# Kernel tuning notes

Hardware: AMD Instinct MI355X
Metric: run time of the kernel (lower is better)

Reference implementation:

```python
import jax, jax.numpy as jnp
import numpy as np

EPS = 1e-12  # torch F.normalize default eps

def _l2_normalize(x):
    # F.normalize(x, dim=1): x / max(||x||_2, eps), per row
    n = jnp.linalg.norm(x, axis=1, keepdims=True)
    return x / jnp.maximum(n, EPS)

def setup_inputs() -> dict:
    key = jax.random.key(0)
    ks = jax.random.split(key, 7)
    B, D = 8192, 4096
    s = 1.0 / np.sqrt(D)  # keep activations well-scaled like nn.Linear init
    return {
        "x":  jax.random.normal(ks[0], (B, D), dtype=jnp.float32),
        "W0": jax.random.normal(ks[1], (D, D), dtype=jnp.float32) * s,
        "b0": jax.random.normal(ks[2], (D,),   dtype=jnp.float32) * s,
        "W1": jax.random.normal(ks[3], (D, D), dtype=jnp.float32) * s,
        "b1": jax.random.normal(ks[4], (D,),   dtype=jnp.float32) * s,
        "W2": jax.random.normal(ks[5], (D, D), dtype=jnp.float32) * s,
        "b2": jax.random.normal(ks[6], (D,),   dtype=jnp.float32) * s,
    }

def reference(x, W0, b0, W1, b1, W2, b2):
    # per layer: out = relu(Linear(l2_normalize(x, dim=1))); collect all layer outputs
    params = [(W0, b0), (W1, b1), (W2, b2)]
    outs = []
    h = x
    for W, b in params:
        hn = _l2_normalize(h)
        # nn.Linear stores weight as [out, in]: y = hn @ W.T + b
        h = jax.nn.relu(jnp.einsum('bi,oi->bo', hn, W) + b)
        outs.append(h)
    return tuple(outs)
```

## Files before the change

### kernel.cpp

```cpp
#include <hip/hip_runtime.h>
#include <hip/hip_bf16.h>


#define NROWS 8192
#define DIM   4096

typedef __bf16 bf16x8 __attribute__((ext_vector_type(8)));
typedef float  f32x4  __attribute__((ext_vector_type(4)));

__device__ static inline short f2bf(float f) {
  __hip_bfloat16 h = __float2bfloat16(f);
  return __builtin_bit_cast(short, h);
}

#define BARRIER() do { asm volatile("" ::: "memory"); \
                       __builtin_amdgcn_s_barrier();  \
                       asm volatile("" ::: "memory"); } while (0)
#define GATE()   do { asm volatile("s_waitcnt lgkmcnt(0)" ::: "memory"); \
                      __builtin_amdgcn_sched_barrier(0); } while (0)
#define VMW(N)   do { asm volatile("s_waitcnt vmcnt(" #N ")" ::: "memory"); \
                      __builtin_amdgcn_sched_barrier(0); } while (0)

__global__ __launch_bounds__(512, 2)
void gemm256_bias_relu(const short* __restrict__ A,
                       const short* __restrict__ Bw,
                       const float* __restrict__ bias,
                       float* __restrict__ C,
                       int M, int N, int K)
{
  __shared__ short lds[5][16384];

  int bid = blockIdx.x;
  const int nwg = gridDim.x;
  if ((nwg & 7) == 0) { const int cpx = nwg >> 3; bid = (bid & 7) * cpx + (bid >> 3); }
  const int nbn  = N >> 8;
  const int brow = (bid / nbn) << 8;
  const int bcol = (bid % nbn) << 8;

  const int lane = threadIdx.x & 63;
  const int wid  = threadIdx.x >> 6;
  const int wr   = wid >> 2;
  const int wc   = wid & 3;

  f32x4 acc[8][4] = {};

  const size_t rowK = (size_t)K * 2;
  char* const  ldsB = (char*)&lds[0][0];

  const int r8  = lane >> 3;
  const int kcs = (lane & 7) ^ r8;
  const char* AgL = (const char*)A  + (size_t)(brow + r8) * rowK + (size_t)kcs * 16;
  const char* BgL = (const char*)Bw + (size_t)(bcol + r8) * rowK + (size_t)kcs * 16;
  int rbo[4], rbb[4];
#pragma unroll
  for (int i = 0; i < 4; ++i) {
    const int rb = wid * 8 + i * 64;
    rbo[i] = rb * (int)rowK;
    rbb[i] = rb * 128;
  }
  auto stage = [&](const char* gsrc, char* lb, int tile) {
    const char* gp = gsrc + ((size_t)tile << 7);
#pragma unroll
    for (int s = 0; s < 4; ++s)
      __builtin_amdgcn_global_load_lds(
          (const __attribute__((address_space(1))) void*)(gp + rbo[s]),
          (__attribute__((address_space(3))) void*)(lb + rbb[s]), 16, 0, 0);
  };

  const int l15  = lane & 15;
  const int xlo  = ((lane >> 4) ^ (lane & 3)) * 16;
  const int b2   = (lane >> 2) & 1;
  const int k64[2] = { b2 << 6, (1 - b2) << 6 };
  const int abase = (wr * 128 + l15) * 128 + xlo;
  const int bbase = (wc * 64  + l15) * 128 + xlo;

  const int NT = K >> 6;

  bf16x8 aX[4][2], aY[4][2], bF[4][2];

#define LOAD_FRAG(DST, PTR, BASE, I0)                                        \
  _Pragma("unroll")                                                          \
  for (int ii = 0; ii < 4; ++ii)                                             \
    _Pragma("unroll")                                                        \
    for (int ks = 0; ks < 2; ++ks)                                           \
      DST[ii][ks] = *reinterpret_cast<const bf16x8*>(                        \
          (PTR) + (BASE) + ((I0) + ii) * 2048 + k64[ks]);

#define MFMA16(I0, AF)                                                       \
  _Pragma("unroll")                                                          \
  for (int ks = 0; ks < 2; ++ks)                                             \
    _Pragma("unroll")                                                        \
    for (int ii = 0; ii < 4; ++ii)                                           \
      _Pragma("unroll")                                                      \
      for (int j = 0; j < 4; ++j)                                            \
        acc[(I0) + ii][j] = __builtin_amdgcn_mfma_f32_16x16x32_bf16(         \
            AF[ii][ks], bF[j][ks], acc[(I0) + ii][j], 0, 0, 0);

  char* a0 = ldsB;
  char* a1 = ldsB + 32768;
  char* a2 = ldsB + 65536;
  char* b0 = ldsB + 98304;
  char* b1 = ldsB + 131072;

  stage(AgL, a0, 0);
  if (NT > 1) stage(AgL, a1, 1);
  stage(BgL, b0, 0);
  if (NT > 1) stage(BgL, b1, 1);
  VMW(0);
  BARRIER();
  LOAD_FRAG(aX, a0, abase, 0)

  for (int t = 0; t < NT; ++t) {
    if (t + 2 < NT) stage(AgL, a2, t + 2);
    LOAD_FRAG(bF, b0, bbase, 0)
    BARRIER();
    GATE();
    LOAD_FRAG(aY, a0, abase, 4)
    __builtin_amdgcn_s_setprio(1);
    MFMA16(0, aX)
    __builtin_amdgcn_s_setprio(0);

    if (t + 2 < NT) { VMW(4); }
    else            { VMW(0); }
    BARRIER();
    GATE();
    if (t + 2 < NT) stage(BgL, b0, t + 2);
    if (t + 1 < NT) { LOAD_FRAG(aX, a1, abase, 0) }
    __builtin_amdgcn_s_setprio(1);
    MFMA16(4, aY)
    __builtin_amdgcn_s_setprio(0);

    char* tmp = a0; a0 = a1; a1 = a2; a2 = tmp;
    char* tb = b0; b0 = b1; b1 = tb;
  }
#undef MFMA16
#undef LOAD_FRAG

  float bv[4];
#pragma unroll
  for (int j = 0; j < 4; ++j)
    bv[j] = bias[bcol + wc * 64 + j * 16 + (lane & 15)];
#pragma unroll
  for (int i = 0; i < 8; ++i) {
    const int rbase = brow + wr * 128 + i * 16 + ((lane >> 4) << 2);
#pragma unroll
    for (int j = 0; j < 4; ++j) {
      const int col = bcol + wc * 64 + j * 16 + (lane & 15);
#pragma unroll
      for (int r = 0; r < 4; ++r) {
        const float v = acc[i][j][r] + bv[j];
        C[(size_t)(rbase + r) * N + col] = v > 0.f ? v : 0.f;
      }
    }
  }
}

__global__ __launch_bounds__(256)
void rownorm_bf16(const float* __restrict__ in, short* __restrict__ out)
{
  const int row = blockIdx.x;
  const int t0  = threadIdx.x;
  const float4* inr = (const float4*)(in + (size_t)row * DIM);

  float4 v[4];
  float ss = 0.f;
#pragma unroll
  for (int t = 0; t < 4; ++t) {
    v[t] = inr[t0 + t * 256];
    ss += v[t].x * v[t].x + v[t].y * v[t].y + v[t].z * v[t].z + v[t].w * v[t].w;
  }
#pragma unroll
  for (int off = 32; off > 0; off >>= 1)
    ss += __shfl_down(ss, off, 64);

  __shared__ float wss[4];
  if ((t0 & 63) == 0) wss[t0 >> 6] = ss;
  __syncthreads();
  const float tot   = wss[0] + wss[1] + wss[2] + wss[3];
  const float scale = 1.f / fmaxf(sqrtf(tot), 1e-12f);

  short4* outr = (short4*)(out + (size_t)row * DIM);
#pragma unroll
  for (int t = 0; t < 4; ++t) {
    short4 o;
    o.x = f2bf(v[t].x * scale);
    o.y = f2bf(v[t].y * scale);
    o.z = f2bf(v[t].z * scale);
    o.w = f2bf(v[t].w * scale);
    outr[t0 + t * 256] = o;
  }
}

__global__ __launch_bounds__(256)
void cast_bf16(const float* __restrict__ in, short* __restrict__ out, int n4)
{
  int i = blockIdx.x * 256 + threadIdx.x;
  const int stride = gridDim.x * 256;
  for (; i < n4; i += stride) {
    const float4 v = ((const float4*)in)[i];
    short4 o;
    o.x = f2bf(v.x);
    o.y = f2bf(v.y);
    o.z = f2bf(v.z);
    o.w = f2bf(v.w);
    ((short4*)out)[i] = o;
  }
}

extern "C" void kernel_launch(void* const* d_in, const int* in_sizes, int n_in,
                              void* d_out, int out_size, void* d_ws, size_t ws_size,
                              hipStream_t stream) {
  const float* x = (const float*)d_in[0];
  const float* W[3]    = { (const float*)d_in[1], (const float*)d_in[3], (const float*)d_in[5] };
  const float* bias[3] = { (const float*)d_in[2], (const float*)d_in[4], (const float*)d_in[6] };
  float* out = (float*)d_out;

  short* hn = (short*)d_ws;
  short* Wb = (short*)((char*)d_ws + (size_t)NROWS * DIM * 2);

  const size_t layer_elems = (size_t)NROWS * DIM;
  const float* hin = x;

  for (int L = 0; L < 3; ++L) {
    cast_bf16<<<2048, 256, 0, stream>>>(W[L], Wb, DIM * DIM / 4);
    rownorm_bf16<<<NROWS, 256, 0, stream>>>(hin, hn);
    gemm256_bias_relu<<<(NROWS / 256) * (DIM / 256), 512, 0, stream>>>(
        hn, Wb, bias[L], out + (size_t)L * layer_elems, NROWS, DIM, DIM);
    hin = out + (size_t)L * layer_elems;
  }
}
```

Before: 807.8 us.

## Shrink GEMM tile to 128x128 with 4 waves and double-buffered LDS

Replaces the 256x256 tile with 8 waves and a triple/double-buffered A/B LDS scheme by a 128x128 tile with 4 waves and a simple double buffer of combined A+B stages. This raises the block count to 2048 and cuts LDS use, aiming for more resident blocks and better load balance across CUs. In exchange arithmetic intensity per tile halves, so global/L2 traffic doubles. Prefetch is now only one stage ahead, with a full vmcnt(0) wait each iteration.

```diff
diff --git a/kernel.cpp b/kernel.cpp
--- a/kernel.cpp
+++ b/kernel.cpp
@@ -21,28 +21,28 @@
 #define VMW(N)   do { asm volatile("s_waitcnt vmcnt(" #N ")" ::: "memory"); \
                       __builtin_amdgcn_sched_barrier(0); } while (0)
 
-__global__ __launch_bounds__(512, 2)
-void gemm256_bias_relu(const short* __restrict__ A,
+__global__ __launch_bounds__(256, 2)
+void gemm128_bias_relu(const short* __restrict__ A,
                        const short* __restrict__ Bw,
                        const float* __restrict__ bias,
                        float* __restrict__ C,
                        int M, int N, int K)
 {
-  __shared__ short lds[5][16384];
+  __shared__ short lds[4][8192];
 
   int bid = blockIdx.x;
   const int nwg = gridDim.x;
   if ((nwg & 7) == 0) { const int cpx = nwg >> 3; bid = (bid & 7) * cpx + (bid >> 3); }
-  const int nbn  = N >> 8;
-  const int brow = (bid / nbn) << 8;
-  const int bcol = (bid % nbn) << 8;
+  const int nbn  = N >> 7;
+  const int brow = (bid / nbn) << 7;
+  const int bcol = (bid % nbn) << 7;
 
   const int lane = threadIdx.x & 63;
   const int wid  = threadIdx.x >> 6;
-  const int wr   = wid >> 2;
-  const int wc   = wid & 3;
-
-  f32x4 acc[8][4] = {};
+  const int wr   = wid >> 1;
+  const int wc   = wid & 1;
+
+  f32x4 acc[4][4] = {};
 
   const size_t rowK = (size_t)K * 2;
   char* const  ldsB = (char*)&lds[0][0];
@@ -54,7 +54,7 @@
   int rbo[4], rbb[4];
 #pragma unroll
   for (int i = 0; i < 4; ++i) {
-    const int rb = wid * 8 + i * 64;
+    const int rb = wid * 8 + i * 32;
     rbo[i] = rb * (int)rowK;
     rbb[i] = rb * 128;
   }
@@ -71,78 +71,74 @@
   const int xlo  = ((lane >> 4) ^ (lane & 3)) * 16;
   const int b2   = (lane >> 2) & 1;
   const int k64[2] = { b2 << 6, (1 - b2) << 6 };
-  const int abase = (wr * 128 + l15) * 128 + xlo;
-  const int bbase = (wc * 64  + l15) * 128 + xlo;
+  const int abase = (wr * 64 + l15) * 128 + xlo;
+  const int bbase = (wc * 64 + l15) * 128 + xlo;
 
   const int NT = K >> 6;
 
-  bf16x8 aX[4][2], aY[4][2], bF[4][2];
-
-#define LOAD_FRAG(DST, PTR, BASE, I0)                                        \
+  bf16x8 aX[2][2], aY[2][2], bF[4][2];
+
+#define LOAD_A2(DST, PTR, I0)                                                \
   _Pragma("unroll")                                                          \
-  for (int ii = 0; ii < 4; ++ii)                                             \
+  for (int ii = 0; ii < 2; ++ii)                                             \
     _Pragma("unroll")                                                        \
     for (int ks = 0; ks < 2; ++ks)                                           \
       DST[ii][ks] = *reinterpret_cast<const bf16x8*>(                        \
-          (PTR) + (BASE) + ((I0) + ii) * 2048 + k64[ks]);
+          (PTR) + abase + ((I0) + ii) * 2048 + k64[ks]);
 
 #define MFMA16(I0, AF)                                                       \
   _Pragma("unroll")                                                          \
   for (int ks = 0; ks < 2; ++ks)                                             \
     _Pragma("unroll")                                                        \
-    for (int ii = 0; ii < 4; ++ii)                                           \
+    for (int ii = 0; ii < 2; ++ii)                                           \
       _Pragma("unroll")                                                      \
       for (int j = 0; j < 4; ++j)                                            \
         acc[(I0) + ii][j] = __builtin_amdgcn_mfma_f32_16x16x32_bf16(         \
             AF[ii][ks], bF[j][ks], acc[(I0) + ii][j], 0, 0, 0);
 
-  char* a0 = ldsB;
-  char* a1 = ldsB + 32768;
-  char* a2 = ldsB + 65536;
-  char* b0 = ldsB + 98304;
-  char* b1 = ldsB + 131072;
-
-  stage(AgL, a0, 0);
-  if (NT > 1) stage(AgL, a1, 1);
-  stage(BgL, b0, 0);
-  if (NT > 1) stage(BgL, b1, 1);
+  stage(AgL, ldsB,         0);
+  stage(BgL, ldsB + 16384, 0);
   VMW(0);
   BARRIER();
-  LOAD_FRAG(aX, a0, abase, 0)
+  LOAD_A2(aX, ldsB, 0)
 
   for (int t = 0; t < NT; ++t) {
-    if (t + 2 < NT) stage(AgL, a2, t + 2);
-    LOAD_FRAG(bF, b0, bbase, 0)
+    const int cur = t & 1;
+    const char* At = ldsB + cur * 32768;
+    const char* Bt = At + 16384;
+    char*       An = ldsB + (cur ^ 1) * 32768;
+
+#pragma unroll
+    for (int j = 0; j < 4; ++j)
+#pragma unroll
+      for (int ks = 0; ks < 2; ++ks)
+        bF[j][ks] = *reinterpret_cast<const bf16x8*>(Bt + bbase + j * 2048 + k64[ks]);
     BARRIER();
+    if (t + 1 < NT) { stage(AgL, An, t + 1); stage(BgL, An + 16384, t + 1); }
     GATE();
-    LOAD_FRAG(aY, a0, abase, 4)
+    LOAD_A2(aY, At, 2)
     __builtin_amdgcn_s_setprio(1);
     MFMA16(0, aX)
     __builtin_amdgcn_s_setprio(0);
 
-    if (t + 2 < NT) { VMW(4); }
-    else            { VMW(0); }
+    VMW(0);
     BARRIER();
     GATE();
-    if (t + 2 < NT) stage(BgL, b0, t + 2);
-    if (t + 1 < NT) { LOAD_FRAG(aX, a1, abase, 0) }
+    if (t + 1 < NT) { LOAD_A2(aX, An, 0) }
     __builtin_amdgcn_s_setprio(1);
-    MFMA16(4, aY)
+    MFMA16(2, aY)
     __builtin_amdgcn_s_setprio(0);
-
-    char* tmp = a0; a0 = a1; a1 = a2; a2 = tmp;
-    char* tb = b0; b0 = b1; b1 = tb;
   }
 #undef MFMA16
-#undef LOAD_FRAG
+#undef LOAD_A2
 
   float bv[4];
 #pragma unroll
   for (int j = 0; j < 4; ++j)
     bv[j] = bias[bcol + wc * 64 + j * 16 + (lane & 15)];
 #pragma unroll
-  for (int i = 0; i < 8; ++i) {
-    const int rbase = brow + wr * 128 + i * 16 + ((lane >> 4) << 2);
+  for (int i = 0; i < 4; ++i) {
+    const int rbase = brow + wr * 64 + i * 16 + ((lane >> 4) << 2);
 #pragma unroll
     for (int j = 0; j < 4; ++j) {
       const int col = bcol + wc * 64 + j * 16 + (lane & 15);
@@ -224,7 +220,7 @@
   for (int L = 0; L < 3; ++L) {
     cast_bf16<<<2048, 256, 0, stream>>>(W[L], Wb, DIM * DIM / 4);
     rownorm_bf16<<<NROWS, 256, 0, stream>>>(hin, hn);
-    gemm256_bias_relu<<<(NROWS / 256) * (DIM / 256), 512, 0, stream>>>(
+    gemm128_bias_relu<<<(NROWS / 128) * (DIM / 128), 256, 0, stream>>>(
         hn, Wb, bias[L], out + (size_t)L * layer_elems, NROWS, DIM, DIM);
     hin = out + (size_t)L * layer_elems;
   }
```

Result: slower. 969.4 us (+20.0%).
